# Performance work log

Hardware: AMD Instinct MI355X
Metric: run time of the kernel (lower is better)

Reference implementation:

```python
import jax, jax.numpy as jnp
import numpy as np

K_SIZE = 5


def extract_patches(x, k):
    """tf.image.extract_patches(SAME, stride 1) -> [B, H, W, k*k, C].

    Kernel offsets are ordered row-major (ki, kj), matching TF's depth
    ordering (ki, kj, c) after the reshape in the original module.
    """
    pad = k // 2
    B, H, W, C = x.shape
    xp = jnp.pad(x, ((0, 0), (pad, pad), (pad, pad), (0, 0)))
    slices = [xp[:, i:i + H, j:j + W, :] for i in range(k) for j in range(k)]
    return jnp.stack(slices, axis=3)  # [B, H, W, k*k, C]


def setup_inputs() -> dict:
    key = jax.random.key(0)
    k1, k2, k3, k4, k5 = jax.random.split(key, 5)
    B, H, C, BIN = 4, 128, 128, 64
    return {
        "main": jax.random.normal(k1, (B, H, H, C), dtype=jnp.float32),
        "ref": jax.random.normal(k2, (B, H, H, C), dtype=jnp.float32),
        "ref_value": jax.random.normal(k3, (B, H, H, BIN), dtype=jnp.float32),
        "W_main": jax.random.normal(k4, (C, C), dtype=jnp.float32) * (2.0 / C) ** 0.5,
        "W_ref": jax.random.normal(k5, (C, C), dtype=jnp.float32) * (2.0 / C) ** 0.5,
    }


def reference(main, ref, ref_value, W_main, W_ref):
    k = K_SIZE
    # 1x1 convolutions (no bias) == per-pixel matmul
    conv_main = jnp.einsum('bhwc,cd->bhwd', main, W_main)
    conv_ref = jnp.einsum('bhwc,cd->bhwd', ref, W_ref)
    # local k x k neighborhood of keys: [B, H, W, k*k, C]
    ref_stacked = extract_patches(conv_ref, k)
    # dot-product attention over the local window
    attn = jnp.einsum('bhwc,bhwkc->bhwk', conv_main, ref_stacked)
    attn = jax.nn.softmax(attn, axis=-1)
    # local k x k neighborhood of values: [B, H, W, k*k, bin]
    ref_value_stacked = extract_patches(ref_value, k)
    # weighted sum of values
    return jnp.einsum('bhwk,bhwki->bhwi', attn, ref_value_stacked)
```

## Files before the change

### kernel.cpp

```cpp
#include <hip/hip_runtime.h>

#define BATCH 4
#define HH 128
#define WW 128
#define CC 128
#define BIN 64
#define NPIX (BATCH * HH * WW)

typedef short bf16x8 __attribute__((ext_vector_type(8)));
typedef float f32x4 __attribute__((ext_vector_type(4)));

__device__ __forceinline__ unsigned bf_hi(float f) {
    unsigned u = __float_as_uint(f);
    return (u + 0x7fffu + ((u >> 16) & 1u)) >> 16;
}
__device__ __forceinline__ uint2 split_aa(float f) {
    unsigned hb = bf_hi(f);
    float lo = f - __uint_as_float(hb << 16);
    unsigned lb = bf_hi(lo);
    return make_uint2(hb | (hb << 16), lb | (lb << 16));
}
__device__ __forceinline__ unsigned split_b(float f) {
    unsigned hb = bf_hi(f);
    float lo = f - __uint_as_float(hb << 16);
    unsigned lb = bf_hi(lo);
    return hb | (lb << 16);
}

#define AROW 72

__global__ __launch_bounds__(256, 3)
void conv_mfma_kernel(const float* __restrict__ Xm, const float* __restrict__ Xr,
                      const float* __restrict__ Wm, const float* __restrict__ Wr,
                      float* __restrict__ Ym, float* __restrict__ Yr) {
    const float* __restrict__ X = blockIdx.y ? Xr : Xm;
    const float* __restrict__ W = blockIdx.y ? Wr : Wm;
    float* __restrict__ Y       = blockIdx.y ? Yr : Ym;

    __shared__ unsigned short AT[128 * AROW];
    __shared__ unsigned short BT[128 * AROW];

    const int t  = threadIdx.x;
    const int wv = t >> 6;
    const int l  = t & 63;
    const int wm = (wv >> 1) * 64;
    const int wn = (wv & 1) * 64;
    const int lr = l & 15;
    const int lq = l >> 4;
    const int p_base = blockIdx.x * 128;

    const int px = t >> 1, ahalf = t & 1;
    const int d  = t & 127, bq = t >> 7;

    f32x4 acc[4][4] = {};

    for (int kc = 0; kc < CC; kc += 16) {
        __syncthreads();
        {
            const float* xp = X + (size_t)(p_base + px) * CC + kc + ahalf * 8;
            unsigned short* arow = &AT[px * AROW + ahalf * 32];
#pragma unroll
            for (int i = 0; i < 2; ++i) {
                float4 v = *(const float4*)(xp + 4 * i);
                uint2 a0 = split_aa(v.x), a1 = split_aa(v.y),
                      a2 = split_aa(v.z), a3 = split_aa(v.w);
                *(uint4*)(arow + 16 * i)     = make_uint4(a0.x, a0.y, a1.x, a1.y);
                *(uint4*)(arow + 16 * i + 8) = make_uint4(a2.x, a2.y, a3.x, a3.y);
            }
        }
        {
#pragma unroll
            for (int j = 0; j < 2; ++j) {
                const int cg = bq * 2 + j;
                const float* wp = W + (size_t)(kc + cg * 4) * CC + d;
                unsigned b0 = split_b(wp[0]);
                unsigned b1 = split_b(wp[CC]);
                unsigned b2 = split_b(wp[2 * CC]);
                unsigned b3 = split_b(wp[3 * CC]);
                unsigned short* brow = &BT[d * AROW + cg * 16];
                *(uint4*)(brow)     = make_uint4(b0, b0, b1, b1);
                *(uint4*)(brow + 8) = make_uint4(b2, b2, b3, b3);
            }
        }
        __syncthreads();
#pragma unroll
        for (int ks = 0; ks < 2; ++ks) {
            bf16x8 af[4], bfr[4];
#pragma unroll
            for (int mi = 0; mi < 4; ++mi)
                af[mi] = *(const bf16x8*)&AT[(wm + mi * 16 + lr) * AROW + ks * 32 + lq * 8];
#pragma unroll
            for (int ni = 0; ni < 4; ++ni)
                bfr[ni] = *(const bf16x8*)&BT[(wn + ni * 16 + lr) * AROW + ks * 32 + lq * 8];
#pragma unroll
            for (int mi = 0; mi < 4; ++mi)
#pragma unroll
                for (int ni = 0; ni < 4; ++ni)
                    acc[mi][ni] = __builtin_amdgcn_mfma_f32_16x16x32_bf16(
                        af[mi], bfr[ni], acc[mi][ni], 0, 0, 0);
        }
    }

#pragma unroll
    for (int mi = 0; mi < 4; ++mi)
#pragma unroll
        for (int ni = 0; ni < 4; ++ni)
#pragma unroll
            for (int reg = 0; reg < 4; ++reg) {
                const int row = p_base + wm + mi * 16 + lq * 4 + reg;
                Y[(size_t)row * CC + wn + ni * 16 + lr] = acc[mi][ni][reg];
            }
}

#define TH 8
#define TW 16
#define HALO_W 20
#define HPX 240
#define NSLOT 1920

__global__ __launch_bounds__(128, 1)
void attn_tile_kernel(const float* __restrict__ qm, const float* __restrict__ kr,
                      const float* __restrict__ vv, float* __restrict__ out) {
    __shared__ float4 KS[2][NSLOT];

    const int t   = threadIdx.x;
    const int wid = t >> 6;
    const int ln  = t & 63;

    const int bi = blockIdx.x >> 7;
    const int ty = (blockIdx.x >> 3) & 15;
    const int tx = blockIdx.x & 7;
    const int h0 = ty * TH, w0 = tx * TW;
    const int r = t >> 4, c = t & 15;
    const int h = h0 + r, w = w0 + c;
    const int gbase = bi * HH * WW;
    const int pix = gbase + h * WW + w;

    unsigned vm = 0;
#pragma unroll
    for (int dy = 0; dy < 5; ++dy)
#pragma unroll
        for (int dx = 0; dx < 5; ++dx) {
            const int hh = h + dy - 2, ww = w + dx - 2;
            if ((unsigned)hh < (unsigned)HH && (unsigned)ww < (unsigned)WW)
                vm |= 1u << (dy * 5 + dx);
        }

    auto stage = [&](int p, int buf) {
        const float* src = (p < 4) ? kr : vv;
        const int ld = (p < 4) ? CC : BIN;
        const int ch = (p < 4) ? p * 32 : (p - 4) * 32;
        for (int i = wid; i < NSLOT / 64; i += 2) {
            const int s   = i * 64 + ln;
            const int g   = s / HPX;
            const int px  = s - g * HPX;
            const int py  = px / HALO_W;
            const int pxx = px - py * HALO_W;
            int hh = h0 + py - 2;  hh = hh < 0 ? 0 : (hh > HH - 1 ? HH - 1 : hh);
            int ww = w0 + pxx - 2; ww = ww < 0 ? 0 : (ww > WW - 1 ? WW - 1 : ww);
            const float* gp = src + (size_t)(gbase + hh * WW + ww) * ld + ch + g * 4;
            __builtin_amdgcn_global_load_lds(
                (const __attribute__((address_space(1))) void*)gp,
                (__attribute__((address_space(3))) void*)&KS[buf][i * 64],
                16, 0, 0);
        }
    };

    float lg[25];
#pragma unroll
    for (int i = 0; i < 25; ++i) lg[i] = 0.0f;

    stage(0, 0);
    __syncthreads();

    for (int p = 0; p < 6; ++p) {
        if (p < 5) stage(p + 1, (p + 1) & 1);
        const float4* B = KS[p & 1];
        if (p < 4) {
            float4 q[8];
            const float4* qp = (const float4*)(qm + (size_t)pix * CC + p * 32);
#pragma unroll
            for (int g = 0; g < 8; ++g) q[g] = qp[g];
#pragma unroll
            for (int dy = 0; dy < 5; ++dy)
#pragma unroll
                for (int dx = 0; dx < 5; ++dx) {
                    const int hp = (r + dy) * HALO_W + (c + dx);
                    float part = 0.0f;
#pragma unroll
                    for (int g = 0; g < 8; ++g) {
                        float4 kv = B[g * HPX + hp];
                        part += q[g].x * kv.x + q[g].y * kv.y +
                                q[g].z * kv.z + q[g].w * kv.w;
                    }
                    lg[dy * 5 + dx] += part;
                }
        } else {
            if (p == 4) {
#pragma unroll
                for (int kk = 0; kk < 25; ++kk)
                    if (!((vm >> kk) & 1)) lg[kk] = 0.0f;
                float mx = lg[0];
#pragma unroll
                for (int kk = 1; kk < 25; ++kk) mx = fmaxf(mx, lg[kk]);
                float sum = 0.0f;
#pragma unroll
                for (int kk = 0; kk < 25; ++kk) {
                    lg[kk] = __expf(lg[kk] - mx);
                    sum += lg[kk];
                }
                const float inv = 1.0f / sum;
#pragma unroll
                for (int kk = 0; kk < 25; ++kk)
                    lg[kk] = ((vm >> kk) & 1) ? lg[kk] * inv : 0.0f;
            }
            float4 va[8];
#pragma unroll
            for (int g = 0; g < 8; ++g) va[g] = make_float4(0.f, 0.f, 0.f, 0.f);
#pragma unroll
            for (int dy = 0; dy < 5; ++dy)
#pragma unroll
                for (int dx = 0; dx < 5; ++dx) {
                    const float wgt = lg[dy * 5 + dx];
                    const int hp = (r + dy) * HALO_W + (c + dx);
#pragma unroll
                    for (int g = 0; g < 8; ++g) {
                        float4 v = B[g * HPX + hp];
                        va[g].x += wgt * v.x; va[g].y += wgt * v.y;
                        va[g].z += wgt * v.z; va[g].w += wgt * v.w;
                    }
                }
            float4* op = (float4*)(out + (size_t)pix * BIN + (p - 4) * 32);
#pragma unroll
            for (int g = 0; g < 8; ++g) op[g] = va[g];
        }
        __syncthreads();
    }
}

extern "C" void kernel_launch(void* const* d_in, const int* in_sizes, int n_in,
                              void* d_out, int out_size, void* d_ws, size_t ws_size,
                              hipStream_t stream) {
    const float* main_in   = (const float*)d_in[0];
    const float* ref_in    = (const float*)d_in[1];
    const float* ref_value = (const float*)d_in[2];
    const float* W_main    = (const float*)d_in[3];
    const float* W_ref     = (const float*)d_in[4];
    float* out = (float*)d_out;

    float* conv_main = (float*)d_ws;
    float* conv_ref  = conv_main + (size_t)NPIX * CC;

    dim3 gconv(NPIX / 128, 2);
    conv_mfma_kernel<<<gconv, 256, 0, stream>>>(main_in, ref_in, W_main, W_ref,
                                                conv_main, conv_ref);

    attn_tile_kernel<<<512, 128, 0, stream>>>(conv_main, conv_ref, ref_value, out);
}
```

Before: 193.9 us.

## Presplit weights, double-buffer conv A tiles, two-row attention threads with 16-channel phases

A new pre-pass splits the weights into hi/lo bf16 pairs once and writes them into the output buffer as scratch. The conv kernel then reads B fragments straight from global memory, double-buffers the A tile in LDS and prefetches the next X chunk, which removes one barrier per k-step. The attention kernel now uses 64-thread blocks where each thread handles two vertically adjacent pixels. This reuses each loaded key/value across both pixels through a 6-row sweep, and streams channels in 16-wide phases with smaller LDS buffers. The risks are more registers per thread, fewer waves per tile, and relying on the output buffer staying untouched until the attention kernel overwrites it.

```diff
diff --git a/kernel.cpp b/kernel.cpp
--- a/kernel.cpp
+++ b/kernel.cpp
@@ -20,25 +20,34 @@
     unsigned lb = bf_hi(lo);
     return make_uint2(hb | (hb << 16), lb | (lb << 16));
 }
-__device__ __forceinline__ unsigned split_b(float f) {
-    unsigned hb = bf_hi(f);
-    float lo = f - __uint_as_float(hb << 16);
-    unsigned lb = bf_hi(lo);
-    return hb | (lb << 16);
+
+__global__ void presplit_w_kernel(const float* __restrict__ Wm,
+                                  const float* __restrict__ Wr,
+                                  unsigned short* __restrict__ WS) {
+    const int t = blockIdx.x * 256 + threadIdx.x;
+    const int conv = t >> 14;
+    const int d = (t >> 7) & 127;
+    const int c = t & 127;
+    const float* W = conv ? Wr : Wm;
+    const float f = W[c * CC + d];
+    const unsigned hb = bf_hi(f);
+    const float lo = f - __uint_as_float(hb << 16);
+    const unsigned lb = bf_hi(lo);
+    const unsigned pk = hb | (lb << 16);
+    *(uint2*)(WS + ((size_t)conv * 128 + d) * 512 + c * 4) = make_uint2(pk, pk);
 }
 
 #define AROW 72
 
 __global__ __launch_bounds__(256, 3)
 void conv_mfma_kernel(const float* __restrict__ Xm, const float* __restrict__ Xr,
-                      const float* __restrict__ Wm, const float* __restrict__ Wr,
+                      const unsigned short* __restrict__ Wsplit,
                       float* __restrict__ Ym, float* __restrict__ Yr) {
     const float* __restrict__ X = blockIdx.y ? Xr : Xm;
-    const float* __restrict__ W = blockIdx.y ? Wr : Wm;
-    float* __restrict__ Y       = blockIdx.y ? Yr : Ym;
-
-    __shared__ unsigned short AT[128 * AROW];
-    __shared__ unsigned short BT[128 * AROW];
+    const unsigned short* __restrict__ WS = Wsplit + (size_t)blockIdx.y * 128 * 512;
+    float* __restrict__ Y = blockIdx.y ? Yr : Ym;
+
+    __shared__ unsigned short AT[2][128 * AROW];
 
     const int t  = threadIdx.x;
     const int wv = t >> 6;
@@ -48,56 +57,51 @@
     const int lr = l & 15;
     const int lq = l >> 4;
     const int p_base = blockIdx.x * 128;
-
     const int px = t >> 1, ahalf = t & 1;
-    const int d  = t & 127, bq = t >> 7;
 
     f32x4 acc[4][4] = {};
 
-    for (int kc = 0; kc < CC; kc += 16) {
+    const float* xbase = X + (size_t)(p_base + px) * CC + ahalf * 8;
+    float4 pa0 = *(const float4*)(xbase);
+    float4 pa1 = *(const float4*)(xbase + 4);
+
+    for (int k = 0; k < 8; ++k) {
+        {
+            unsigned short* arow = &AT[k & 1][px * AROW + ahalf * 32];
+            uint2 a0 = split_aa(pa0.x), a1 = split_aa(pa0.y),
+                  a2 = split_aa(pa0.z), a3 = split_aa(pa0.w);
+            *(uint4*)(arow)     = make_uint4(a0.x, a0.y, a1.x, a1.y);
+            *(uint4*)(arow + 8) = make_uint4(a2.x, a2.y, a3.x, a3.y);
+            uint2 b0 = split_aa(pa1.x), b1 = split_aa(pa1.y),
+                  b2 = split_aa(pa1.z), b3 = split_aa(pa1.w);
+            *(uint4*)(arow + 16) = make_uint4(b0.x, b0.y, b1.x, b1.y);
+            *(uint4*)(arow + 24) = make_uint4(b2.x, b2.y, b3.x, b3.y);
+        }
         __syncthreads();
-        {
-            const float* xp = X + (size_t)(p_base + px) * CC + kc + ahalf * 8;
-            unsigned short* arow = &AT[px * AROW + ahalf * 32];
-#pragma unroll
-            for (int i = 0; i < 2; ++i) {
-                float4 v = *(const float4*)(xp + 4 * i);
-                uint2 a0 = split_aa(v.x), a1 = split_aa(v.y),
-                      a2 = split_aa(v.z), a3 = split_aa(v.w);
-                *(uint4*)(arow + 16 * i)     = make_uint4(a0.x, a0.y, a1.x, a1.y);
-                *(uint4*)(arow + 16 * i + 8) = make_uint4(a2.x, a2.y, a3.x, a3.y);
-            }
-        }
-        {
-#pragma unroll
-            for (int j = 0; j < 2; ++j) {
-                const int cg = bq * 2 + j;
-                const float* wp = W + (size_t)(kc + cg * 4) * CC + d;
-                unsigned b0 = split_b(wp[0]);
-                unsigned b1 = split_b(wp[CC]);
-                unsigned b2 = split_b(wp[2 * CC]);
-                unsigned b3 = split_b(wp[3 * CC]);
-                unsigned short* brow = &BT[d * AROW + cg * 16];
-                *(uint4*)(brow)     = make_uint4(b0, b0, b1, b1);
-                *(uint4*)(brow + 8) = make_uint4(b2, b2, b3, b3);
-            }
-        }
-        __syncthreads();
+        if (k < 7) {
+            const float* xp = xbase + (k + 1) * 16;
+            pa0 = *(const float4*)(xp);
+            pa1 = *(const float4*)(xp + 4);
+        }
+        bf16x8 bfr[2][4];
+#pragma unroll
+        for (int ks = 0; ks < 2; ++ks)
+#pragma unroll
+            for (int ni = 0; ni < 4; ++ni)
+                bfr[ks][ni] = *(const bf16x8*)(
+                    WS + (size_t)(wn + ni * 16 + lr) * 512 + k * 64 + ks * 32 + lq * 8);
 #pragma unroll
         for (int ks = 0; ks < 2; ++ks) {
-            bf16x8 af[4], bfr[4];
+            bf16x8 af[4];
 #pragma unroll
             for (int mi = 0; mi < 4; ++mi)
-                af[mi] = *(const bf16x8*)&AT[(wm + mi * 16 + lr) * AROW + ks * 32 + lq * 8];
-#pragma unroll
-            for (int ni = 0; ni < 4; ++ni)
-                bfr[ni] = *(const bf16x8*)&BT[(wn + ni * 16 + lr) * AROW + ks * 32 + lq * 8];
+                af[mi] = *(const bf16x8*)&AT[k & 1][(wm + mi * 16 + lr) * AROW + ks * 32 + lq * 8];
 #pragma unroll
             for (int mi = 0; mi < 4; ++mi)
 #pragma unroll
                 for (int ni = 0; ni < 4; ++ni)
                     acc[mi][ni] = __builtin_amdgcn_mfma_f32_16x16x32_bf16(
-                        af[mi], bfr[ni], acc[mi][ni], 0, 0, 0);
+                        af[mi], bfr[ks][ni], acc[mi][ni], 0, 0, 0);
         }
     }
 
@@ -112,49 +116,52 @@
             }
 }
 
-#define TH 8
-#define TW 16
+#define T_W 16
+#define T_H 8
 #define HALO_W 20
 #define HPX 240
-#define NSLOT 1920
-
-__global__ __launch_bounds__(128, 1)
-void attn_tile_kernel(const float* __restrict__ qm, const float* __restrict__ kr,
-                      const float* __restrict__ vv, float* __restrict__ out) {
-    __shared__ float4 KS[2][NSLOT];
-
-    const int t   = threadIdx.x;
-    const int wid = t >> 6;
-    const int ln  = t & 63;
-
+#define CH_SLOTS (HPX * 4)
+
+__global__ __launch_bounds__(64, 2)
+void attn_kernel(const float* __restrict__ qm, const float* __restrict__ kr,
+                 const float* __restrict__ vv, float* __restrict__ out) {
+    __shared__ float4 KS[2][CH_SLOTS];
+
+    const int t  = threadIdx.x;
     const int bi = blockIdx.x >> 7;
-    const int ty = (blockIdx.x >> 3) & 15;
-    const int tx = blockIdx.x & 7;
-    const int h0 = ty * TH, w0 = tx * TW;
-    const int r = t >> 4, c = t & 15;
-    const int h = h0 + r, w = w0 + c;
+    const int tile = blockIdx.x & 127;
+    const int ty = tile >> 3;
+    const int tx = tile & 7;
+    const int h0 = ty * T_H, w0 = tx * T_W;
+    const int c = t & 15;
+    const int r = (t >> 4) * 2;
     const int gbase = bi * HH * WW;
-    const int pix = gbase + h * WW + w;
-
-    unsigned vm = 0;
+    const int pix0 = gbase + (h0 + r) * WW + (w0 + c);
+    const int pix1 = pix0 + WW;
+
+    unsigned vm0 = 0, vm1 = 0;
 #pragma unroll
     for (int dy = 0; dy < 5; ++dy)
 #pragma unroll
         for (int dx = 0; dx < 5; ++dx) {
-            const int hh = h + dy - 2, ww = w + dx - 2;
-            if ((unsigned)hh < (unsigned)HH && (unsigned)ww < (unsigned)WW)
-                vm |= 1u << (dy * 5 + dx);
-        }
-
-    auto stage = [&](int p, int buf) {
-        const float* src = (p < 4) ? kr : vv;
-        const int ld = (p < 4) ? CC : BIN;
-        const int ch = (p < 4) ? p * 32 : (p - 4) * 32;
-        for (int i = wid; i < NSLOT / 64; i += 2) {
-            const int s   = i * 64 + ln;
-            const int g   = s / HPX;
-            const int px  = s - g * HPX;
-            const int py  = px / HALO_W;
+            const int ww = w0 + c + dx - 2;
+            const bool cok = (unsigned)ww < (unsigned)WW;
+            const int h_a = h0 + r + dy - 2;
+            const int h_b = h_a + 1;
+            if (cok && (unsigned)h_a < (unsigned)HH) vm0 |= 1u << (dy * 5 + dx);
+            if (cok && (unsigned)h_b < (unsigned)HH) vm1 |= 1u << (dy * 5 + dx);
+        }
+
+    auto stage = [&](int phase, int buf) {
+        const float* src = (phase < 8) ? kr : vv;
+        const int ld = (phase < 8) ? CC : BIN;
+        const int ch = (phase < 8) ? phase * 16 : (phase - 8) * 16;
+#pragma unroll
+        for (int i = 0; i < 15; ++i) {
+            const int s  = i * 64 + t;
+            const int g  = s / HPX;
+            const int px = s - g * HPX;
+            const int py = px / HALO_W;
             const int pxx = px - py * HALO_W;
             int hh = h0 + py - 2;  hh = hh < 0 ? 0 : (hh > HH - 1 ? HH - 1 : hh);
             int ww = w0 + pxx - 2; ww = ww < 0 ? 0 : (ww > WW - 1 ? WW - 1 : ww);
@@ -166,75 +173,103 @@
         }
     };
 
-    float lg[25];
-#pragma unroll
-    for (int i = 0; i < 25; ++i) lg[i] = 0.0f;
+    float lg0[25], lg1[25];
+#pragma unroll
+    for (int i = 0; i < 25; ++i) { lg0[i] = 0.0f; lg1[i] = 0.0f; }
 
     stage(0, 0);
-    __syncthreads();
-
-    for (int p = 0; p < 6; ++p) {
-        if (p < 5) stage(p + 1, (p + 1) & 1);
+
+    for (int p = 0; p < 8; ++p) {
+        __syncthreads();
+        stage(p + 1, (p + 1) & 1);
+        float4 q0[4], q1[4];
+        {
+            const float4* qp0 = (const float4*)(qm + (size_t)pix0 * CC + p * 16);
+            const float4* qp1 = (const float4*)(qm + (size_t)pix1 * CC + p * 16);
+#pragma unroll
+            for (int g = 0; g < 4; ++g) { q0[g] = qp0[g]; q1[g] = qp1[g]; }
+        }
         const float4* B = KS[p & 1];
-        if (p < 4) {
-            float4 q[8];
-            const float4* qp = (const float4*)(qm + (size_t)pix * CC + p * 32);
-#pragma unroll
-            for (int g = 0; g < 8; ++g) q[g] = qp[g];
-#pragma unroll
-            for (int dy = 0; dy < 5; ++dy)
-#pragma unroll
-                for (int dx = 0; dx < 5; ++dx) {
-                    const int hp = (r + dy) * HALO_W + (c + dx);
-                    float part = 0.0f;
-#pragma unroll
-                    for (int g = 0; g < 8; ++g) {
-                        float4 kv = B[g * HPX + hp];
-                        part += q[g].x * kv.x + q[g].y * kv.y +
-                                q[g].z * kv.z + q[g].w * kv.w;
+#pragma unroll
+        for (int dy2 = 0; dy2 < 6; ++dy2) {
+            const int hbase = (r + dy2) * HALO_W + c;
+#pragma unroll
+            for (int dx = 0; dx < 5; ++dx) {
+                const int hp = hbase + dx;
+#pragma unroll
+                for (int g = 0; g < 4; ++g) {
+                    float4 kv = B[g * HPX + hp];
+                    if (dy2 < 5)
+                        lg0[dy2 * 5 + dx] += q0[g].x * kv.x + q0[g].y * kv.y +
+                                             q0[g].z * kv.z + q0[g].w * kv.w;
+                    if (dy2 >= 1)
+                        lg1[(dy2 - 1) * 5 + dx] += q1[g].x * kv.x + q1[g].y * kv.y +
+                                                   q1[g].z * kv.z + q1[g].w * kv.w;
+                }
+            }
+        }
+    }
+
+    {
+#pragma unroll
+        for (int kk = 0; kk < 25; ++kk) {
+            if (!((vm0 >> kk) & 1)) lg0[kk] = 0.0f;
+            if (!((vm1 >> kk) & 1)) lg1[kk] = 0.0f;
+        }
+        float m0 = lg0[0], m1 = lg1[0];
+#pragma unroll
+        for (int kk = 1; kk < 25; ++kk) { m0 = fmaxf(m0, lg0[kk]); m1 = fmaxf(m1, lg1[kk]); }
+        float s0 = 0.0f, s1 = 0.0f;
+#pragma unroll
+        for (int kk = 0; kk < 25; ++kk) {
+            lg0[kk] = __expf(lg0[kk] - m0); s0 += lg0[kk];
+            lg1[kk] = __expf(lg1[kk] - m1); s1 += lg1[kk];
+        }
+        const float i0 = 1.0f / s0, i1 = 1.0f / s1;
+#pragma unroll
+        for (int kk = 0; kk < 25; ++kk) {
+            lg0[kk] = ((vm0 >> kk) & 1) ? lg0[kk] * i0 : 0.0f;
+            lg1[kk] = ((vm1 >> kk) & 1) ? lg1[kk] * i1 : 0.0f;
+        }
+    }
+
+    for (int p = 8; p < 12; ++p) {
+        __syncthreads();
+        if (p < 11) stage(p + 1, (p + 1) & 1);
+        const float4* B = KS[p & 1];
+        float4 va0[4], va1[4];
+#pragma unroll
+        for (int g = 0; g < 4; ++g) {
+            va0[g] = make_float4(0.f, 0.f, 0.f, 0.f);
+            va1[g] = make_float4(0.f, 0.f, 0.f, 0.f);
+        }
+#pragma unroll
+        for (int dy2 = 0; dy2 < 6; ++dy2) {
+            const int hbase = (r + dy2) * HALO_W + c;
+#pragma unroll
+            for (int dx = 0; dx < 5; ++dx) {
+                const int hp = hbase + dx;
+                const float w_0 = (dy2 < 5) ? lg0[dy2 * 5 + dx] : 0.0f;
+                const float w_1 = (dy2 >= 1) ? lg1[(dy2 - 1) * 5 + dx] : 0.0f;
+#pragma unroll
+                for (int g = 0; g < 4; ++g) {
+                    float4 kv = B[g * HPX + hp];
+                    if (dy2 < 5) {
+                        va0[g].x += w_0 * kv.x; va0[g].y += w_0 * kv.y;
+                        va0[g].z += w_0 * kv.z; va0[g].w += w_0 * kv.w;
                     }
-                    lg[dy * 5 + dx] += part;
-                }
-        } else {
-            if (p == 4) {
-#pragma unroll
-                for (int kk = 0; kk < 25; ++kk)
-                    if (!((vm >> kk) & 1)) lg[kk] = 0.0f;
-                float mx = lg[0];
-#pragma unroll
-                for (int kk = 1; kk < 25; ++kk) mx = fmaxf(mx, lg[kk]);
-                float sum = 0.0f;
-#pragma unroll
-                for (int kk = 0; kk < 25; ++kk) {
-                    lg[kk] = __expf(lg[kk] - mx);
-                    sum += lg[kk];
-                }
-                const float inv = 1.0f / sum;
-#pragma unroll
-                for (int kk = 0; kk < 25; ++kk)
-                    lg[kk] = ((vm >> kk) & 1) ? lg[kk] * inv : 0.0f;
-            }
-            float4 va[8];
-#pragma unroll
-            for (int g = 0; g < 8; ++g) va[g] = make_float4(0.f, 0.f, 0.f, 0.f);
-#pragma unroll
-            for (int dy = 0; dy < 5; ++dy)
-#pragma unroll
-                for (int dx = 0; dx < 5; ++dx) {
-                    const float wgt = lg[dy * 5 + dx];
-                    const int hp = (r + dy) * HALO_W + (c + dx);
-#pragma unroll
-                    for (int g = 0; g < 8; ++g) {
-                        float4 v = B[g * HPX + hp];
-                        va[g].x += wgt * v.x; va[g].y += wgt * v.y;
-                        va[g].z += wgt * v.z; va[g].w += wgt * v.w;
+                    if (dy2 >= 1) {
+                        va1[g].x += w_1 * kv.x; va1[g].y += w_1 * kv.y;
+                        va1[g].z += w_1 * kv.z; va1[g].w += w_1 * kv.w;
                     }
                 }
-            float4* op = (float4*)(out + (size_t)pix * BIN + (p - 4) * 32);
-#pragma unroll
-            for (int g = 0; g < 8; ++g) op[g] = va[g];
-        }
-        __syncthreads();
+            }
+        }
+        const int ch = (p - 8) * 16;
+        float4* op0 = (float4*)(out + (size_t)pix0 * BIN + ch);
+        float4* op1 = (float4*)(out + (size_t)pix1 * BIN + ch);
+#pragma unroll
+        for (int g = 0; g < 4; ++g) { op0[g] = va0[g]; op1[g] = va1[g]; }
     }
 }
 
@@ -250,10 +285,13 @@
 
     float* conv_main = (float*)d_ws;
     float* conv_ref  = conv_main + (size_t)NPIX * CC;
+    unsigned short* WS = (unsigned short*)d_out;
+
+    presplit_w_kernel<<<128, 256, 0, stream>>>(W_main, W_ref, WS);
 
     dim3 gconv(NPIX / 128, 2);
-    conv_mfma_kernel<<<gconv, 256, 0, stream>>>(main_in, ref_in, W_main, W_ref,
+    conv_mfma_kernel<<<gconv, 256, 0, stream>>>(main_in, ref_in, WS,
                                                 conv_main, conv_ref);
 
-    attn_tile_kernel<<<512, 128, 0, stream>>>(conv_main, conv_ref, ref_value, out);
-}
+    attn_kernel<<<512, 64, 0, stream>>>(conv_main, conv_ref, ref_value, out);
+}
```

After: 214.4 us. +10.6%, slower.

## Presplit weights, shrink conv tiles, and retile attention into 8x8 blocks

Applied to the files above, without the earlier changes.

Adds a small kernel that splits both weight matrices into bf16 hi/lo pairs once, writing them into the output buffer as scratch. The conv kernel now reads those pre-split weights directly from global memory, uses 64-pixel tiles with a double-buffered activation tile and register prefetch, and targets higher occupancy. The attention kernel moves to 8x8 pixel tiles with two threads per pixel splitting channels. It uses a single smaller LDS buffer so more blocks fit per CU, and combines partial logits with a lane shuffle. This trades the old double-buffered overlap for more blocks in flight and a smaller halo footprint per block, at the cost of extra barriers and more halo redundancy.

```diff
diff --git a/kernel.cpp b/kernel.cpp
--- a/kernel.cpp
+++ b/kernel.cpp
@@ -20,89 +20,84 @@
     unsigned lb = bf_hi(lo);
     return make_uint2(hb | (hb << 16), lb | (lb << 16));
 }
-__device__ __forceinline__ unsigned split_b(float f) {
-    unsigned hb = bf_hi(f);
-    float lo = f - __uint_as_float(hb << 16);
-    unsigned lb = bf_hi(lo);
-    return hb | (lb << 16);
+
+__global__ void presplit_w_kernel(const float* __restrict__ Wm,
+                                  const float* __restrict__ Wr,
+                                  unsigned short* __restrict__ WS) {
+    const int t = blockIdx.x * 256 + threadIdx.x;
+    const int conv = t >> 14;
+    const int d = (t >> 7) & 127;
+    const int c = t & 127;
+    const float* W = conv ? Wr : Wm;
+    const float f = W[c * CC + d];
+    const unsigned hb = bf_hi(f);
+    const float lo = f - __uint_as_float(hb << 16);
+    const unsigned lb = bf_hi(lo);
+    const unsigned pk = hb | (lb << 16);
+    *(uint2*)(WS + ((size_t)conv * 128 + d) * 512 + c * 4) = make_uint2(pk, pk);
 }
 
 #define AROW 72
 
-__global__ __launch_bounds__(256, 3)
+__global__ __launch_bounds__(256, 4)
 void conv_mfma_kernel(const float* __restrict__ Xm, const float* __restrict__ Xr,
-                      const float* __restrict__ Wm, const float* __restrict__ Wr,
+                      const unsigned short* __restrict__ Wsplit,
                       float* __restrict__ Ym, float* __restrict__ Yr) {
     const float* __restrict__ X = blockIdx.y ? Xr : Xm;
-    const float* __restrict__ W = blockIdx.y ? Wr : Wm;
-    float* __restrict__ Y       = blockIdx.y ? Yr : Ym;
-
-    __shared__ unsigned short AT[128 * AROW];
-    __shared__ unsigned short BT[128 * AROW];
+    const unsigned short* __restrict__ WS = Wsplit + (size_t)blockIdx.y * 128 * 512;
+    float* __restrict__ Y = blockIdx.y ? Yr : Ym;
+
+    __shared__ unsigned short AT[2][64 * AROW];
 
     const int t  = threadIdx.x;
     const int wv = t >> 6;
     const int l  = t & 63;
-    const int wm = (wv >> 1) * 64;
-    const int wn = (wv & 1) * 64;
     const int lr = l & 15;
     const int lq = l >> 4;
-    const int p_base = blockIdx.x * 128;
-
-    const int px = t >> 1, ahalf = t & 1;
-    const int d  = t & 127, bq = t >> 7;
-
-    f32x4 acc[4][4] = {};
-
-    for (int kc = 0; kc < CC; kc += 16) {
-        __syncthreads();
+    const int wm = (wv & 1) * 32;
+    const int wn = (wv >> 1) * 64;
+    const int p_base = blockIdx.x * 64;
+    const int px = t >> 2, q = t & 3;
+
+    f32x4 acc[2][4] = {};
+
+    const float* xptr = X + (size_t)(p_base + px) * CC + q * 4;
+    float4 pa = *(const float4*)xptr;
+
+    for (int k = 0; k < 8; ++k) {
         {
-            const float* xp = X + (size_t)(p_base + px) * CC + kc + ahalf * 8;
-            unsigned short* arow = &AT[px * AROW + ahalf * 32];
-#pragma unroll
-            for (int i = 0; i < 2; ++i) {
-                float4 v = *(const float4*)(xp + 4 * i);
-                uint2 a0 = split_aa(v.x), a1 = split_aa(v.y),
-                      a2 = split_aa(v.z), a3 = split_aa(v.w);
-                *(uint4*)(arow + 16 * i)     = make_uint4(a0.x, a0.y, a1.x, a1.y);
-                *(uint4*)(arow + 16 * i + 8) = make_uint4(a2.x, a2.y, a3.x, a3.y);
-            }
-        }
-        {
-#pragma unroll
-            for (int j = 0; j < 2; ++j) {
-                const int cg = bq * 2 + j;
-                const float* wp = W + (size_t)(kc + cg * 4) * CC + d;
-                unsigned b0 = split_b(wp[0]);
-                unsigned b1 = split_b(wp[CC]);
-                unsigned b2 = split_b(wp[2 * CC]);
-                unsigned b3 = split_b(wp[3 * CC]);
-                unsigned short* brow = &BT[d * AROW + cg * 16];
-                *(uint4*)(brow)     = make_uint4(b0, b0, b1, b1);
-                *(uint4*)(brow + 8) = make_uint4(b2, b2, b3, b3);
-            }
-        }
-        __syncthreads();
+            unsigned short* arow = &AT[k & 1][px * AROW + q * 16];
+            uint2 a0 = split_aa(pa.x), a1 = split_aa(pa.y),
+                  a2 = split_aa(pa.z), a3 = split_aa(pa.w);
+            *(uint4*)(arow)     = make_uint4(a0.x, a0.y, a1.x, a1.y);
+            *(uint4*)(arow + 8) = make_uint4(a2.x, a2.y, a3.x, a3.y);
+        }
+        if (k < 7) pa = *(const float4*)(xptr + (k + 1) * 16);
+        __syncthreads();
+        bf16x8 bfr[2][4];
+#pragma unroll
+        for (int ks = 0; ks < 2; ++ks)
+#pragma unroll
+            for (int ni = 0; ni < 4; ++ni)
+                bfr[ks][ni] = *(const bf16x8*)(
+                    WS + (size_t)(wn + ni * 16 + lr) * 512 + k * 64 + ks * 32 + lq * 8);
 #pragma unroll
         for (int ks = 0; ks < 2; ++ks) {
-            bf16x8 af[4], bfr[4];
-#pragma unroll
-            for (int mi = 0; mi < 4; ++mi)
-                af[mi] = *(const bf16x8*)&AT[(wm + mi * 16 + lr) * AROW + ks * 32 + lq * 8];
-#pragma unroll
-            for (int ni = 0; ni < 4; ++ni)
-                bfr[ni] = *(const bf16x8*)&BT[(wn + ni * 16 + lr) * AROW + ks * 32 + lq * 8];
-#pragma unroll
-            for (int mi = 0; mi < 4; ++mi)
+            bf16x8 af[2];
+#pragma unroll
+            for (int mi = 0; mi < 2; ++mi)
+                af[mi] = *(const bf16x8*)&AT[k & 1][(wm + mi * 16 + lr) * AROW + ks * 32 + lq * 8];
+#pragma unroll
+            for (int mi = 0; mi < 2; ++mi)
 #pragma unroll
                 for (int ni = 0; ni < 4; ++ni)
                     acc[mi][ni] = __builtin_amdgcn_mfma_f32_16x16x32_bf16(
-                        af[mi], bfr[ni], acc[mi][ni], 0, 0, 0);
-        }
-    }
-
-#pragma unroll
-    for (int mi = 0; mi < 4; ++mi)
+                        af[mi], bfr[ks][ni], acc[mi][ni], 0, 0, 0);
+        }
+    }
+
+#pragma unroll
+    for (int mi = 0; mi < 2; ++mi)
 #pragma unroll
         for (int ni = 0; ni < 4; ++ni)
 #pragma unroll
@@ -112,56 +107,63 @@
             }
 }
 
-#define TH 8
-#define TW 16
-#define HALO_W 20
-#define HPX 240
-#define NSLOT 1920
-
-__global__ __launch_bounds__(128, 1)
-void attn_tile_kernel(const float* __restrict__ qm, const float* __restrict__ kr,
-                      const float* __restrict__ vv, float* __restrict__ out) {
-    __shared__ float4 KS[2][NSLOT];
+#define HGRP 156
+#define HSTR 628
+#define KSLOTS 1280
+
+__global__ __launch_bounds__(128, 3)
+void attn_kernel(const float* __restrict__ qm, const float* __restrict__ kr,
+                 const float* __restrict__ vv, float* __restrict__ out) {
+    __shared__ float4 KS[KSLOTS];
 
     const int t   = threadIdx.x;
     const int wid = t >> 6;
     const int ln  = t & 63;
-
-    const int bi = blockIdx.x >> 7;
-    const int ty = (blockIdx.x >> 3) & 15;
-    const int tx = blockIdx.x & 7;
-    const int h0 = ty * TH, w0 = tx * TW;
-    const int r = t >> 4, c = t & 15;
-    const int h = h0 + r, w = w0 + c;
+    const int bx  = blockIdx.x;
+    const int bi  = bx >> 8;
+    const int ty  = (bx >> 4) & 15;
+    const int tx  = bx & 15;
+    const int h0 = ty * 8, w0 = tx * 8;
+
+    const int p    = t >> 1;
+    const int half = t & 1;
+    const int r = p >> 3, c = p & 7;
     const int gbase = bi * HH * WW;
-    const int pix = gbase + h * WW + w;
+    const int pix = gbase + (h0 + r) * WW + (w0 + c);
 
     unsigned vm = 0;
 #pragma unroll
     for (int dy = 0; dy < 5; ++dy)
 #pragma unroll
         for (int dx = 0; dx < 5; ++dx) {
-            const int hh = h + dy - 2, ww = w + dx - 2;
+            const int hh = h0 + r + dy - 2, ww = w0 + c + dx - 2;
             if ((unsigned)hh < (unsigned)HH && (unsigned)ww < (unsigned)WW)
                 vm |= 1u << (dy * 5 + dx);
         }
 
-    auto stage = [&](int p, int buf) {
-        const float* src = (p < 4) ? kr : vv;
-        const int ld = (p < 4) ? CC : BIN;
-        const int ch = (p < 4) ? p * 32 : (p - 4) * 32;
-        for (int i = wid; i < NSLOT / 64; i += 2) {
-            const int s   = i * 64 + ln;
-            const int g   = s / HPX;
-            const int px  = s - g * HPX;
-            const int py  = px / HALO_W;
-            const int pxx = px - py * HALO_W;
+    auto stage = [&](int phase) {
+        const float* src = (phase < 4) ? kr : vv;
+        const int ld  = (phase < 4) ? CC : BIN;
+        const int chb = (phase < 4) ? phase * 32 : (phase - 4) * 32;
+#pragma unroll
+        for (int i = 0; i < 10; ++i) {
+            const int base_slot = i * 128 + wid * 64;
+            int s = base_slot + ln;
+            if (s > 1255) s = 1255;
+            const int hr = s / HSTR;
+            int rem = s - hr * HSTR;
+            if (rem > 623) rem = 623;
+            const int g    = hr * 4 + rem / HGRP;
+            const int rem2 = rem % HGRP;
+            const int py   = rem2 / 13;
+            int pxx = rem2 - py * 13;
+            if (pxx > 11) pxx = 11;
             int hh = h0 + py - 2;  hh = hh < 0 ? 0 : (hh > HH - 1 ? HH - 1 : hh);
             int ww = w0 + pxx - 2; ww = ww < 0 ? 0 : (ww > WW - 1 ? WW - 1 : ww);
-            const float* gp = src + (size_t)(gbase + hh * WW + ww) * ld + ch + g * 4;
+            const float* gp = src + (size_t)(gbase + hh * WW + ww) * ld + chb + g * 4;
             __builtin_amdgcn_global_load_lds(
                 (const __attribute__((address_space(1))) void*)gp,
-                (__attribute__((address_space(3))) void*)&KS[buf][i * 64],
+                (__attribute__((address_space(3))) void*)&KS[base_slot],
                 16, 0, 0);
         }
     };
@@ -170,71 +172,82 @@
 #pragma unroll
     for (int i = 0; i < 25; ++i) lg[i] = 0.0f;
 
-    stage(0, 0);
-    __syncthreads();
-
-    for (int p = 0; p < 6; ++p) {
-        if (p < 5) stage(p + 1, (p + 1) & 1);
-        const float4* B = KS[p & 1];
-        if (p < 4) {
-            float4 q[8];
-            const float4* qp = (const float4*)(qm + (size_t)pix * CC + p * 32);
-#pragma unroll
-            for (int g = 0; g < 8; ++g) q[g] = qp[g];
-#pragma unroll
-            for (int dy = 0; dy < 5; ++dy)
-#pragma unroll
-                for (int dx = 0; dx < 5; ++dx) {
-                    const int hp = (r + dy) * HALO_W + (c + dx);
-                    float part = 0.0f;
-#pragma unroll
-                    for (int g = 0; g < 8; ++g) {
-                        float4 kv = B[g * HPX + hp];
-                        part += q[g].x * kv.x + q[g].y * kv.y +
-                                q[g].z * kv.z + q[g].w * kv.w;
-                    }
-                    lg[dy * 5 + dx] += part;
+    stage(0);
+
+    for (int kp = 0; kp < 4; ++kp) {
+        __syncthreads();
+        float4 q4[4];
+        {
+            const float4* qp = (const float4*)(qm + (size_t)pix * CC + kp * 32 + half * 16);
+#pragma unroll
+            for (int gi = 0; gi < 4; ++gi) q4[gi] = qp[gi];
+        }
+        const float4* B = KS + half * HSTR;
+#pragma unroll
+        for (int dy = 0; dy < 5; ++dy)
+#pragma unroll
+            for (int dx = 0; dx < 5; ++dx) {
+                const int hp = (r + dy) * 13 + (c + dx);
+                float part = 0.0f;
+#pragma unroll
+                for (int gi = 0; gi < 4; ++gi) {
+                    float4 kv = B[gi * HGRP + hp];
+                    part += q4[gi].x * kv.x + q4[gi].y * kv.y +
+                            q4[gi].z * kv.z + q4[gi].w * kv.w;
                 }
-        } else {
-            if (p == 4) {
-#pragma unroll
-                for (int kk = 0; kk < 25; ++kk)
-                    if (!((vm >> kk) & 1)) lg[kk] = 0.0f;
-                float mx = lg[0];
-#pragma unroll
-                for (int kk = 1; kk < 25; ++kk) mx = fmaxf(mx, lg[kk]);
-                float sum = 0.0f;
-#pragma unroll
-                for (int kk = 0; kk < 25; ++kk) {
-                    lg[kk] = __expf(lg[kk] - mx);
-                    sum += lg[kk];
+                lg[dy * 5 + dx] += part;
+            }
+        __syncthreads();
+        stage(kp + 1);
+    }
+
+    {
+#pragma unroll
+        for (int kk = 0; kk < 25; ++kk) {
+            lg[kk] += __shfl_xor(lg[kk], 1, 64);
+            if (!((vm >> kk) & 1)) lg[kk] = 0.0f;
+        }
+        float mx = lg[0];
+#pragma unroll
+        for (int kk = 1; kk < 25; ++kk) mx = fmaxf(mx, lg[kk]);
+        float sum = 0.0f;
+#pragma unroll
+        for (int kk = 0; kk < 25; ++kk) {
+            lg[kk] = __expf(lg[kk] - mx);
+            sum += lg[kk];
+        }
+        const float inv = 1.0f / sum;
+#pragma unroll
+        for (int kk = 0; kk < 25; ++kk)
+            lg[kk] = ((vm >> kk) & 1) ? lg[kk] * inv : 0.0f;
+    }
+
+    for (int vp = 0; vp < 2; ++vp) {
+        __syncthreads();
+        const float4* B = KS + half * HSTR;
+        float4 va[4];
+#pragma unroll
+        for (int gi = 0; gi < 4; ++gi) va[gi] = make_float4(0.f, 0.f, 0.f, 0.f);
+#pragma unroll
+        for (int dy = 0; dy < 5; ++dy)
+#pragma unroll
+            for (int dx = 0; dx < 5; ++dx) {
+                const float wgt = lg[dy * 5 + dx];
+                const int hp = (r + dy) * 13 + (c + dx);
+#pragma unroll
+                for (int gi = 0; gi < 4; ++gi) {
+                    float4 v = B[gi * HGRP + hp];
+                    va[gi].x += wgt * v.x; va[gi].y += wgt * v.y;
+                    va[gi].z += wgt * v.z; va[gi].w += wgt * v.w;
                 }
-                const float inv = 1.0f / sum;
-#pragma unroll
-                for (int kk = 0; kk < 25; ++kk)
-                    lg[kk] = ((vm >> kk) & 1) ? lg[kk] * inv : 0.0f;
             }
-            float4 va[8];
-#pragma unroll
-            for (int g = 0; g < 8; ++g) va[g] = make_float4(0.f, 0.f, 0.f, 0.f);
-#pragma unroll
-            for (int dy = 0; dy < 5; ++dy)
-#pragma unroll
-                for (int dx = 0; dx < 5; ++dx) {
-                    const float wgt = lg[dy * 5 + dx];
-                    const int hp = (r + dy) * HALO_W + (c + dx);
-#pragma unroll
-                    for (int g = 0; g < 8; ++g) {
-                        float4 v = B[g * HPX + hp];
-                        va[g].x += wgt * v.x; va[g].y += wgt * v.y;
-                        va[g].z += wgt * v.z; va[g].w += wgt * v.w;
-                    }
-                }
-            float4* op = (float4*)(out + (size_t)pix * BIN + (p - 4) * 32);
-#pragma unroll
-            for (int g = 0; g < 8; ++g) op[g] = va[g];
-        }
-        __syncthreads();
+        float4* op = (float4*)(out + (size_t)pix * BIN + vp * 32 + half * 16);
+#pragma unroll
+        for (int gi = 0; gi < 4; ++gi) op[gi] = va[gi];
+        if (vp == 0) {
+            __syncthreads();
+            stage(5);
+        }
     }
 }
 
@@ -250,10 +263,13 @@
 
     float* conv_main = (float*)d_ws;
     float* conv_ref  = conv_main + (size_t)NPIX * CC;
-
-    dim3 gconv(NPIX / 128, 2);
-    conv_mfma_kernel<<<gconv, 256, 0, stream>>>(main_in, ref_in, W_main, W_ref,
+    unsigned short* WS = (unsigned short*)d_out;
+
+    presplit_w_kernel<<<128, 256, 0, stream>>>(W_main, W_ref, WS);
+
+    dim3 gconv(NPIX / 64, 2);
+    conv_mfma_kernel<<<gconv, 256, 0, stream>>>(main_in, ref_in, WS,
                                                 conv_main, conv_ref);
 
-    attn_tile_kernel<<<512, 128, 0, stream>>>(conv_main, conv_ref, ref_value, out);
-}
+    attn_kernel<<<1024, 128, 0, stream>>>(conv_main, conv_ref, ref_value, out);
+}
```

New measurement: 216.6 us. +11.7%, slower.
